# Optimization experiments

Hardware: AMD Instinct MI355X
Metric: run time of the kernel (lower is better)

## Reference

```python
import jax, jax.numpy as jnp
import numpy as np

B, C, H, W = 8, 256, 64, 64
NUM_HEADS = 4


def setup_inputs() -> dict:
    key = jax.random.key(0)
    ks = jax.random.split(key, 6)
    s = 0.02  # small init scale for 1x1 conv weights
    return {
        "x": jax.random.normal(ks[0], (B, C, H, W), jnp.float32),
        "cproj": jax.random.normal(ks[1], (B, C, H, W), jnp.float32),
        "wq": jax.random.normal(ks[2], (C, C), jnp.float32) * s,
        "bq": jnp.zeros((C,), jnp.float32),
        "wkv": jax.random.normal(ks[3], (2 * C, C), jnp.float32) * s,
        "bkv": jnp.zeros((2 * C,), jnp.float32),
        "wo": jax.random.normal(ks[4], (C, C), jnp.float32) * s,  # zero_module in torch; random here for a meaningful baseline
        "bo": jnp.zeros((C,), jnp.float32),
    }


def reference(x, cproj, wq, bq, wkv, bkv, wo, bo):
    Bb, Cc, Hh, Ww = x.shape
    N = Hh * Ww
    h = NUM_HEADS
    d = Cc // h
    scale = 1.0 / jnp.sqrt(jnp.sqrt(jnp.asarray(Cc, jnp.float32)))

    xf = x.reshape(Bb, Cc, N)
    cf = cproj.reshape(Bb, Cc, N)

    # 1x1 convs == channel matmuls
    Q = jnp.einsum('oc,bcn->bon', wq, xf) + bq[None, :, None]           # (B,C,N)
    KV = jnp.einsum('oc,bcn->bon', wkv, cf) + bkv[None, :, None]        # (B,2C,N)
    K, V = KV[:, :Cc], KV[:, Cc:]

    # softmax over channel-dim-within-head for q, over spatial N for k
    q = jax.nn.softmax(Q.reshape(Bb, h, d, N) * scale, axis=2).reshape(Bb, Cc, N)
    k = jax.nn.softmax(K.reshape(Bb, h, d, N), axis=3).reshape(Bb, Cc, N)

    # linear-attention: (B,C,C) context, then project back to N — note heads are mixed, per original bmm
    context = jnp.einsum('bcn,bdn->bcd', k, V)
    out = jnp.einsum('bcd,bdn->bcn', context, q)

    out = jnp.einsum('oc,bcn->bon', wo, out) + bo[None, :, None]
    return out.reshape(Bb, Cc, Hh, Ww)
```

## Files before the change

kernel.cpp:

```cpp
#include <hip/hip_runtime.h>

#define B_ 8
#define C_ 256
#define N_ 4096
#define NSPLIT 16

typedef float f32x4 __attribute__((ext_vector_type(4)));
typedef __bf16 bf16x8 __attribute__((ext_vector_type(8)));
typedef __bf16 bf16x4 __attribute__((ext_vector_type(4)));
typedef unsigned short u16x8 __attribute__((ext_vector_type(8)));
typedef unsigned short u16x4 __attribute__((ext_vector_type(4)));

__device__ __forceinline__ unsigned short f2bf(float f) {
  return __builtin_bit_cast(unsigned short, (__bf16)f);
}
__device__ __forceinline__ float bf2f(unsigned short u) {
  return __uint_as_float((unsigned)u << 16);
}

__device__ __forceinline__ f32x4 mfma16(bf16x8 a, bf16x8 b, f32x4 c) {
  return __builtin_amdgcn_mfma_f32_16x16x32_bf16(a, b, c, 0, 0, 0);
}

typedef __attribute__((address_space(1))) const void* gvp;
typedef __attribute__((address_space(3))) void* lvp;
__device__ __forceinline__ void gld16(const void* g, void* l) {
  __builtin_amdgcn_global_load_lds((gvp)g, (lvp)l, 16, 0, 0);
}

#define VMWAIT(N) do { asm volatile("s_waitcnt vmcnt(" #N ")" ::: "memory"); \
                       __builtin_amdgcn_sched_barrier(0); } while (0)
#define BAR() __builtin_amdgcn_s_barrier()

template <int ROWS>
__device__ __forceinline__ void stage(unsigned short* lds, const unsigned short* g,
                                      int ld, int w, int lane) {
  const int r8 = lane >> 3;
  const int ce = ((lane & 7) ^ r8) << 3;
  const unsigned short* gp = g + (size_t)(w * (ROWS / 4) + r8) * ld + ce;
  unsigned short* lp = lds + w * (ROWS / 4) * 64;
#pragma unroll
  for (int i = 0; i < ROWS / 32; i++)
    gld16(gp + (size_t)(i * 8) * ld, lp + i * 512);
}

__device__ __forceinline__ bf16x8 frag(const unsigned short* lds, int row, int kc) {
  return *(const bf16x8*)(lds + row * 64 + ((kc ^ (row & 7)) << 3));
}

__device__ __forceinline__ void loadB(float4* pbv, const float* src, int ld,
                                      int n0, int kt, int w, int lane) {
  const int nf = lane & 15, kg = lane >> 4;
  const float* sp = src + (size_t)(kt * 64 + w * 16 + kg * 4) * ld + n0 + 4 * nf;
#pragma unroll
  for (int h = 0; h < 2; h++)
#pragma unroll
    for (int i = 0; i < 4; i++)
      pbv[h * 4 + i] = *(const float4*)(sp + h * 64 + (size_t)i * ld);
}
__device__ __forceinline__ void writeB(unsigned short* Bs, const float4* pbv,
                                       int w, int lane) {
  const int nf = lane & 15, kg = lane >> 4;
  const int k0 = w * 16 + kg * 4;
#pragma unroll
  for (int h = 0; h < 2; h++)
#pragma unroll
    for (int j = 0; j < 4; j++) {
      bf16x4 o = (bf16x4){(__bf16)((const float*)&pbv[h * 4 + 0])[j],
                          (__bf16)((const float*)&pbv[h * 4 + 1])[j],
                          (__bf16)((const float*)&pbv[h * 4 + 2])[j],
                          (__bf16)((const float*)&pbv[h * 4 + 3])[j]};
      *(bf16x4*)&Bs[(h * 64 + 4 * nf + j) * 68 + k0] = o;
    }
}
__device__ __forceinline__ bf16x8 fragB(const unsigned short* Bs, int n, int k8) {
  union { u16x4 q[2]; bf16x8 b; } u;
  const unsigned short* p = Bs + n * 68 + k8 * 8;
  u.q[0] = *(const u16x4*)p;
  u.q[1] = *(const u16x4*)(p + 4);
  return u.b;
}

__device__ __forceinline__ bf16x8 fragC(const unsigned short* Ct, int n, int k8) {
  union { u16x4 q[2]; bf16x8 b; } u;
  const unsigned short* p = Ct + n * 268 + k8 * 8;
  u.q[0] = *(const u16x4*)p;
  u.q[1] = *(const u16x4*)(p + 4);
  return u.b;
}

__global__ __launch_bounds__(256) void castw(
    const float* __restrict__ wq, const float* __restrict__ wkv,
    const float* __restrict__ wo, unsigned short* __restrict__ wqb,
    unsigned short* __restrict__ wkvb, unsigned short* __restrict__ wob,
    float* __restrict__ Z) {
  int t = blockIdx.x * 256 + threadIdx.x;
  if (t < B_ * C_) Z[t] = 0.f;
  int i = t * 4;
  const float* src;
  unsigned short* dst;
  int off;
  if (i < 65536) { src = wq; dst = wqb; off = i; }
  else if (i < 196608) { src = wkv; dst = wkvb; off = i - 65536; }
  else { src = wo; dst = wob; off = i - 196608; }
  float4 v = *(const float4*)(src + off);
  *(u16x4*)(dst + off) = (u16x4){f2bf(v.x), f2bf(v.y), f2bf(v.z), f2bf(v.w)};
}

__device__ __forceinline__ void qproj_body(
    unsigned short* As, unsigned short* Bs, const unsigned short* __restrict__ wqb,
    const float* __restrict__ x, const float* __restrict__ bq,
    unsigned short* __restrict__ qT, int b, int n0, int m0b) {
  const int tid = threadIdx.x, lane = tid & 63, w = tid >> 6;
  const int m0w = (w >> 1) * 64;
  const int n0w = (w & 1) * 64;
  const int colL = lane & 15, kq = lane >> 4, quad = lane >> 4;
  const float* xb = x + (size_t)b * C_ * N_;

  f32x4 acc[4][4];
#pragma unroll
  for (int i = 0; i < 4; i++)
#pragma unroll
    for (int j = 0; j < 4; j++) acc[i][j] = (f32x4){0.f, 0.f, 0.f, 0.f};

  float4 pbv[8];
  loadB(pbv, xb, N_, n0, 0, w, lane);

  for (int kt = 0; kt < 4; kt++) {
    writeB(Bs, pbv, w, lane);
    stage<128>(As, wqb + (size_t)m0b * C_ + kt * 64, C_, w, lane);
    __syncthreads();
    if (kt < 3) loadB(pbv, xb, N_, n0, kt + 1, w, lane);
#pragma unroll
    for (int ks = 0; ks < 2; ks++) {
      bf16x8 af[4], bf[4];
#pragma unroll
      for (int mt = 0; mt < 4; mt++) af[mt] = frag(As, m0w + mt * 16 + colL, ks * 4 + kq);
#pragma unroll
      for (int nt = 0; nt < 4; nt++) bf[nt] = fragB(Bs, n0w + nt * 16 + colL, ks * 4 + kq);
#pragma unroll
      for (int mt = 0; mt < 4; mt++)
#pragma unroll
        for (int nt = 0; nt < 4; nt++) acc[mt][nt] = mfma16(af[mt], bf[nt], acc[mt][nt]);
    }
    __syncthreads();
  }

#pragma unroll
  for (int nt = 0; nt < 4; nt++) {
    float v[16];
    float mx = -1e30f;
#pragma unroll
    for (int mt = 0; mt < 4; mt++)
#pragma unroll
      for (int r = 0; r < 4; r++) {
        int m = m0b + m0w + mt * 16 + quad * 4 + r;
        float val = (acc[mt][nt][r] + bq[m]) * 0.25f;
        v[mt * 4 + r] = val;
        mx = fmaxf(mx, val);
      }
    mx = fmaxf(mx, __shfl_xor(mx, 16));
    mx = fmaxf(mx, __shfl_xor(mx, 32));
    float s = 0.f;
#pragma unroll
    for (int j = 0; j < 16; j++) { v[j] = __expf(v[j] - mx); s += v[j]; }
    s += __shfl_xor(s, 16);
    s += __shfl_xor(s, 32);
    float inv = 1.0f / s;
    const int n = n0 + n0w + nt * 16 + colL;
    unsigned short* qb = qT + ((size_t)b * N_ + n) * C_ + m0b + m0w;
#pragma unroll
    for (int mt = 0; mt < 4; mt++) {
      u16x4 o = (u16x4){f2bf(v[mt * 4 + 0] * inv), f2bf(v[mt * 4 + 1] * inv),
                        f2bf(v[mt * 4 + 2] * inv), f2bf(v[mt * 4 + 3] * inv)};
      *(u16x4*)(qb + mt * 16 + quad * 4) = o;
    }
  }
}

__device__ __forceinline__ void kvproj_body(
    unsigned short* As, unsigned short* Bs, const unsigned short* __restrict__ wkvb,
    const float* __restrict__ cp, const float* __restrict__ bkv,
    unsigned short* __restrict__ Eb, unsigned short* __restrict__ Vb,
    float* __restrict__ Z, int b, int n0, int m0b) {
  const int tid = threadIdx.x, lane = tid & 63, w = tid >> 6;
  const int m0w = w * 32;
  const int colL = lane & 15, kq = lane >> 4, quad = lane >> 4;
  const float* cpb = cp + (size_t)b * C_ * N_;

  f32x4 acc[2][8];
#pragma unroll
  for (int i = 0; i < 2; i++)
#pragma unroll
    for (int j = 0; j < 8; j++) acc[i][j] = (f32x4){0.f, 0.f, 0.f, 0.f};

  float4 pbv[8];
  loadB(pbv, cpb, N_, n0, 0, w, lane);

  for (int kt = 0; kt < 4; kt++) {
    writeB(Bs, pbv, w, lane);
    stage<128>(As, wkvb + (size_t)m0b * C_ + kt * 64, C_, w, lane);
    __syncthreads();
    if (kt < 3) loadB(pbv, cpb, N_, n0, kt + 1, w, lane);
#pragma unroll
    for (int ks = 0; ks < 2; ks++) {
      bf16x8 bf[8];
#pragma unroll
      for (int nt = 0; nt < 8; nt++) bf[nt] = fragB(Bs, nt * 16 + colL, ks * 4 + kq);
#pragma unroll
      for (int mt = 0; mt < 2; mt++) {
        bf16x8 af = frag(As, m0w + mt * 16 + colL, ks * 4 + kq);
#pragma unroll
        for (int nt = 0; nt < 8; nt++) acc[mt][nt] = mfma16(af, bf[nt], acc[mt][nt]);
      }
    }
    __syncthreads();
  }

#pragma unroll
  for (int mt = 0; mt < 2; mt++)
#pragma unroll
    for (int r = 0; r < 4; r++) {
      int m = m0b + m0w + mt * 16 + quad * 4 + r;
      float bias = bkv[m];
      if (m < C_) {
        unsigned short* er = Eb + ((size_t)b * C_ + m) * N_ + n0;
        float es = 0.f;
#pragma unroll
        for (int nt = 0; nt < 8; nt++) {
          float e = __expf(acc[mt][nt][r] + bias);
          er[nt * 16 + colL] = f2bf(e);
          es += e;
        }
        es += __shfl_xor(es, 1);
        es += __shfl_xor(es, 2);
        es += __shfl_xor(es, 4);
        es += __shfl_xor(es, 8);
        if ((lane & 15) == 0) atomicAdd(&Z[b * C_ + m], es);
      } else {
        unsigned short* vr = Vb + ((size_t)b * C_ + m - C_) * N_ + n0;
#pragma unroll
        for (int nt = 0; nt < 8; nt++) vr[nt * 16 + colL] = f2bf(acc[mt][nt][r] + bias);
      }
    }
}

__global__ __launch_bounds__(256) void qkvproj(
    const unsigned short* __restrict__ wqb, const unsigned short* __restrict__ wkvb,
    const float* __restrict__ x, const float* __restrict__ cp,
    const float* __restrict__ bq, const float* __restrict__ bkv,
    unsigned short* __restrict__ qT, unsigned short* __restrict__ Eb,
    unsigned short* __restrict__ Vb, float* __restrict__ Z) {
  __shared__ __align__(16) unsigned short As[128 * 64];
  __shared__ __align__(16) unsigned short Bs[128 * 68];
  const int b = blockIdx.z, n0 = blockIdx.x * 128;
  if (blockIdx.y < 2)
    qproj_body(As, Bs, wqb, x, bq, qT, b, n0, blockIdx.y * 128);
  else
    kvproj_body(As, Bs, wkvb, cp, bkv, Eb, Vb, Z, b, n0, (blockIdx.y - 2) * 128);
}

__global__ __launch_bounds__(256) void ctx_part(
    const unsigned short* __restrict__ Eb, const float* __restrict__ Z,
    const unsigned short* __restrict__ Vb, unsigned short* __restrict__ ctxp) {
  __shared__ __align__(16) unsigned short As[2][128 * 64];
  __shared__ __align__(16) unsigned short Bs[2][128 * 64];
  const int bid = blockIdx.x;
  const int swz = (bid & 7) * 64 + (bid >> 3);
  const int b = swz >> 6, r = swz & 63;
  const int s = r >> 2;
  const int m0 = ((r >> 1) & 1) * 128, n0 = (r & 1) * 128;
  const int tid = threadIdx.x, lane = tid & 63, w = tid >> 6;
  const int m0w = (w & 1) * 64, n0w = (w >> 1) * 64;
  const int colL = lane & 15, kq = lane >> 4, quad = lane >> 4;
  const unsigned short* Ag = Eb + ((size_t)b * C_ + m0) * N_ + s * (N_ / NSPLIT);
  const unsigned short* Bg = Vb + ((size_t)b * C_ + n0) * N_ + s * (N_ / NSPLIT);

  f32x4 acc[4][4];
#pragma unroll
  for (int i = 0; i < 4; i++)
#pragma unroll
    for (int j = 0; j < 4; j++) acc[i][j] = (f32x4){0.f, 0.f, 0.f, 0.f};

  stage<128>(As[0], Ag + 0 * 64, N_, w, lane);
  stage<128>(Bs[0], Bg + 0 * 64, N_, w, lane);
  stage<128>(As[1], Ag + 1 * 64, N_, w, lane);
  stage<128>(Bs[1], Bg + 1 * 64, N_, w, lane);
  VMWAIT(8);
  BAR();

  for (int kt = 0; kt < 4; kt++) {
    const unsigned short* Asc = As[kt & 1];
    const unsigned short* Bsc = Bs[kt & 1];
#pragma unroll
    for (int ks = 0; ks < 2; ks++) {
      bf16x8 af[4], bf[4];
#pragma unroll
      for (int mt = 0; mt < 4; mt++) af[mt] = frag(Asc, m0w + mt * 16 + colL, ks * 4 + kq);
#pragma unroll
      for (int nt = 0; nt < 4; nt++) bf[nt] = frag(Bsc, n0w + nt * 16 + colL, ks * 4 + kq);
#pragma unroll
      for (int mt = 0; mt < 4; mt++)
#pragma unroll
        for (int nt = 0; nt < 4; nt++) acc[mt][nt] = mfma16(af[mt], bf[nt], acc[mt][nt]);
    }
    if (kt == 3) break;
    BAR();
    if (kt + 2 < 4) {
      stage<128>(As[kt & 1], Ag + (kt + 2) * 64, N_, w, lane);
      stage<128>(Bs[kt & 1], Bg + (kt + 2) * 64, N_, w, lane);
      VMWAIT(8);
    } else {
      VMWAIT(0);
    }
    BAR();
  }

  unsigned short* outp = ctxp + ((size_t)s * B_ + b) * C_ * C_;
  const float* Zb = Z + b * C_;
#pragma unroll
  for (int mt = 0; mt < 4; mt++)
#pragma unroll
    for (int r2 = 0; r2 < 4; r2++) {
      int m = m0 + m0w + mt * 16 + quad * 4 + r2;
      float iz = 1.0f / Zb[m];
#pragma unroll
      for (int nt = 0; nt < 4; nt++) {
        int n = n0 + n0w + nt * 16 + colL;
        outp[(size_t)m * C_ + n] = f2bf(acc[mt][nt][r2] * iz);
      }
    }
}

__global__ __launch_bounds__(256) void ctxoproj(
    const unsigned short* __restrict__ ctxp, const unsigned short* __restrict__ wob,
    unsigned short* __restrict__ ctx2) {
  __shared__ __align__(16) unsigned short AsW[4 * 64 * 64];
  __shared__ __align__(16) unsigned short Ct[32 * 268];
  const int bid = blockIdx.x;
  const int swz = (bid & 7) * 32 + (bid >> 3);
  const int b = swz >> 5, r = swz & 31;
  const int o0 = (r >> 3) * 64, d0 = (r & 7) * 32;
  const int tid = threadIdx.x, lane = tid & 63, w = tid >> 6;
  const int colL = lane & 15, kq = lane >> 4, quad = lane >> 4;

#pragma unroll
  for (int ck = 0; ck < 4; ck++)
    stage<64>(AsW + ck * 4096, wob + (size_t)o0 * C_ + ck * 64, C_, w, lane);

  const int q = tid & 7, cl = tid >> 3;
  const unsigned short* pb = ctxp + ((size_t)b * C_ + cl) * C_ + d0 + q * 4;
#pragma unroll 2
  for (int p = 0; p < 8; p++) {
    f32x4 s4 = (f32x4){0.f, 0.f, 0.f, 0.f};
    const unsigned short* pp = pb + (size_t)p * 32 * C_;
#pragma unroll
    for (int s = 0; s < NSPLIT; s++) {
      u16x4 v = *(const u16x4*)(pp + (size_t)s * B_ * C_ * C_);
      s4[0] += bf2f(v[0]); s4[1] += bf2f(v[1]);
      s4[2] += bf2f(v[2]); s4[3] += bf2f(v[3]);
    }
    const int c = p * 32 + cl;
#pragma unroll
    for (int j = 0; j < 4; j++) Ct[(q * 4 + j) * 268 + c] = f2bf(s4[j]);
  }
  __syncthreads();

  f32x4 acc2[2];
  acc2[0] = (f32x4){0.f, 0.f, 0.f, 0.f};
  acc2[1] = (f32x4){0.f, 0.f, 0.f, 0.f};
#pragma unroll
  for (int kt = 0; kt < 4; kt++)
#pragma unroll
    for (int ks = 0; ks < 2; ks++) {
      bf16x8 af = frag(AsW + kt * 4096, w * 16 + colL, ks * 4 + kq);
#pragma unroll
      for (int nt = 0; nt < 2; nt++) {
        bf16x8 bf = fragC(Ct, nt * 16 + colL, kt * 8 + ks * 4 + kq);
        acc2[nt] = mfma16(af, bf, acc2[nt]);
      }
    }
  unsigned short* ob = ctx2 + (size_t)b * C_ * C_;
#pragma unroll
  for (int nt = 0; nt < 2; nt++)
#pragma unroll
    for (int r2 = 0; r2 < 4; r2++)
      ob[(size_t)(o0 + w * 16 + quad * 4 + r2) * C_ + d0 + nt * 16 + colL] =
          f2bf(acc2[nt][r2]);
}

__global__ __launch_bounds__(256) void outgemm(
    const unsigned short* __restrict__ ctx2, const unsigned short* __restrict__ qT,
    const float* __restrict__ bo, float* __restrict__ out) {
  __shared__ __align__(16) unsigned short As[2][128 * 64];
  __shared__ __align__(16) unsigned short Bs[2][64 * 64];
  const int bid = blockIdx.x;
  const int swz = (bid & 7) * 128 + (bid >> 3);
  const int b = swz >> 7, r = swz & 127;
  const int m0b = (r >> 6) * 128, n0 = (r & 63) * 64;
  const int tid = threadIdx.x, lane = tid & 63, w = tid >> 6;
  const int m0w = w * 32;
  const int colL = lane & 15, kq = lane >> 4, quad = lane >> 4;
  const unsigned short* Ag = ctx2 + (size_t)b * C_ * C_ + (size_t)m0b * C_;
  const unsigned short* Bg = qT + ((size_t)b * N_ + n0) * C_;

  f32x4 acc[2][4];
#pragma unroll
  for (int i = 0; i < 2; i++)
#pragma unroll
    for (int j = 0; j < 4; j++) acc[i][j] = (f32x4){0.f, 0.f, 0.f, 0.f};

  stage<128>(As[0], Ag + 0 * 64, C_, w, lane);
  stage<64>(Bs[0], Bg + 0 * 64, C_, w, lane);
  stage<128>(As[1], Ag + 1 * 64, C_, w, lane);
  stage<64>(Bs[1], Bg + 1 * 64, C_, w, lane);
  VMWAIT(6);
  BAR();

  for (int kt = 0; kt < 4; kt++) {
    const unsigned short* Asc = As[kt & 1];
    const unsigned short* Bsc = Bs[kt & 1];
#pragma unroll
    for (int ks = 0; ks < 2; ks++) {
      bf16x8 af[2], bf[4];
#pragma unroll
      for (int mt = 0; mt < 2; mt++) af[mt] = frag(Asc, m0w + mt * 16 + colL, ks * 4 + kq);
#pragma unroll
      for (int nt = 0; nt < 4; nt++) bf[nt] = frag(Bsc, nt * 16 + colL, ks * 4 + kq);
#pragma unroll
      for (int mt = 0; mt < 2; mt++)
#pragma unroll
        for (int nt = 0; nt < 4; nt++) acc[mt][nt] = mfma16(af[mt], bf[nt], acc[mt][nt]);
    }
    if (kt == 3) break;
    BAR();
    if (kt + 2 < 4) {
      stage<128>(As[kt & 1], Ag + (kt + 2) * 64, C_, w, lane);
      stage<64>(Bs[kt & 1], Bg + (kt + 2) * 64, C_, w, lane);
      VMWAIT(6);
    } else {
      VMWAIT(0);
    }
    BAR();
  }

  float* ob = out + (size_t)b * C_ * N_;
#pragma unroll
  for (int mt = 0; mt < 2; mt++)
#pragma unroll
    for (int r2 = 0; r2 < 4; r2++) {
      int m = m0b + m0w + mt * 16 + quad * 4 + r2;
      float bias = bo[m];
#pragma unroll
      for (int nt = 0; nt < 4; nt++) {
        int n = n0 + nt * 16 + colL;
        ob[(size_t)m * N_ + n] = acc[mt][nt][r2] + bias;
      }
    }
}

extern "C" void kernel_launch(void* const* d_in, const int* in_sizes, int n_in,
                              void* d_out, int out_size, void* d_ws, size_t ws_size,
                              hipStream_t stream) {
  const float* x     = (const float*)d_in[0];
  const float* cproj = (const float*)d_in[1];
  const float* wq    = (const float*)d_in[2];
  const float* bq    = (const float*)d_in[3];
  const float* wkv   = (const float*)d_in[4];
  const float* bkv   = (const float*)d_in[5];
  const float* wo    = (const float*)d_in[6];
  const float* bo    = (const float*)d_in[7];
  float* out = (float*)d_out;

  unsigned short* qT    = (unsigned short*)d_ws;
  unsigned short* Eb    = qT + 8388608;
  unsigned short* Vb    = Eb + 8388608;
  unsigned short* ctxp  = Vb + 8388608;
  unsigned short* wqb   = ctxp + 8388608;
  unsigned short* wkvb  = wqb + 65536;
  unsigned short* wob   = wkvb + 131072;
  unsigned short* ctx2  = wob + 65536;
  float*          Zbuf  = (float*)(ctx2 + 524288);

  castw<<<256, 256, 0, stream>>>(wq, wkv, wo, wqb, wkvb, wob, Zbuf);
  qkvproj<<<dim3(32, 6, 8), 256, 0, stream>>>(wqb, wkvb, x, cproj, bq, bkv,
                                              qT, Eb, Vb, Zbuf);
  ctx_part<<<512, 256, 0, stream>>>(Eb, Zbuf, Vb, ctxp);
  ctxoproj<<<256, 256, 0, stream>>>(ctxp, wob, ctx2);
  outgemm<<<1024, 256, 0, stream>>>(ctx2, qT, bo, out);
}
```

Measured before the change: 181.4 us.

## Move Q projection into the context kernel to overlap with ctx partials

Splits the fused QKV projection launch into a KV-only projection and a new kernel that runs the context partial GEMM blocks alongside the Q projection blocks. The goal is to fill the GPU during the context stage, which has only 512 blocks, with the independent Q projection work, and to shorten the KV kernel. In exchange the ctx body gives up its double-buffered async staging for a simple single-buffer loop with syncthreads, so it shares the same LDS footprint with qproj. The B-tile LDS pitch also changes from 68 to 70 to alter the bank-conflict pattern.

```diff
diff --git a/kernel.cpp b/kernel.cpp
--- a/kernel.cpp
+++ b/kernel.cpp
@@ -48,6 +48,7 @@
   return *(const bf16x8*)(lds + row * 64 + ((kc ^ (row & 7)) << 3));
 }
 
+#define BPITCH 70
 __device__ __forceinline__ void loadB(float4* pbv, const float* src, int ld,
                                       int n0, int kt, int w, int lane) {
   const int nf = lane & 15, kg = lane >> 4;
@@ -70,12 +71,12 @@
                           (__bf16)((const float*)&pbv[h * 4 + 1])[j],
                           (__bf16)((const float*)&pbv[h * 4 + 2])[j],
                           (__bf16)((const float*)&pbv[h * 4 + 3])[j]};
-      *(bf16x4*)&Bs[(h * 64 + 4 * nf + j) * 68 + k0] = o;
+      *(bf16x4*)&Bs[(h * 64 + 4 * nf + j) * BPITCH + k0] = o;
     }
 }
 __device__ __forceinline__ bf16x8 fragB(const unsigned short* Bs, int n, int k8) {
   union { u16x4 q[2]; bf16x8 b; } u;
-  const unsigned short* p = Bs + n * 68 + k8 * 8;
+  const unsigned short* p = Bs + n * BPITCH + k8 * 8;
   u.q[0] = *(const u16x4*)p;
   u.q[1] = *(const u16x4*)(p + 4);
   return u.b;
@@ -107,77 +108,6 @@
   *(u16x4*)(dst + off) = (u16x4){f2bf(v.x), f2bf(v.y), f2bf(v.z), f2bf(v.w)};
 }
 
-__device__ __forceinline__ void qproj_body(
-    unsigned short* As, unsigned short* Bs, const unsigned short* __restrict__ wqb,
-    const float* __restrict__ x, const float* __restrict__ bq,
-    unsigned short* __restrict__ qT, int b, int n0, int m0b) {
-  const int tid = threadIdx.x, lane = tid & 63, w = tid >> 6;
-  const int m0w = (w >> 1) * 64;
-  const int n0w = (w & 1) * 64;
-  const int colL = lane & 15, kq = lane >> 4, quad = lane >> 4;
-  const float* xb = x + (size_t)b * C_ * N_;
-
-  f32x4 acc[4][4];
-#pragma unroll
-  for (int i = 0; i < 4; i++)
-#pragma unroll
-    for (int j = 0; j < 4; j++) acc[i][j] = (f32x4){0.f, 0.f, 0.f, 0.f};
-
-  float4 pbv[8];
-  loadB(pbv, xb, N_, n0, 0, w, lane);
-
-  for (int kt = 0; kt < 4; kt++) {
-    writeB(Bs, pbv, w, lane);
-    stage<128>(As, wqb + (size_t)m0b * C_ + kt * 64, C_, w, lane);
-    __syncthreads();
-    if (kt < 3) loadB(pbv, xb, N_, n0, kt + 1, w, lane);
-#pragma unroll
-    for (int ks = 0; ks < 2; ks++) {
-      bf16x8 af[4], bf[4];
-#pragma unroll
-      for (int mt = 0; mt < 4; mt++) af[mt] = frag(As, m0w + mt * 16 + colL, ks * 4 + kq);
-#pragma unroll
-      for (int nt = 0; nt < 4; nt++) bf[nt] = fragB(Bs, n0w + nt * 16 + colL, ks * 4 + kq);
-#pragma unroll
-      for (int mt = 0; mt < 4; mt++)
-#pragma unroll
-        for (int nt = 0; nt < 4; nt++) acc[mt][nt] = mfma16(af[mt], bf[nt], acc[mt][nt]);
-    }
-    __syncthreads();
-  }
-
-#pragma unroll
-  for (int nt = 0; nt < 4; nt++) {
-    float v[16];
-    float mx = -1e30f;
-#pragma unroll
-    for (int mt = 0; mt < 4; mt++)
-#pragma unroll
-      for (int r = 0; r < 4; r++) {
-        int m = m0b + m0w + mt * 16 + quad * 4 + r;
-        float val = (acc[mt][nt][r] + bq[m]) * 0.25f;
-        v[mt * 4 + r] = val;
-        mx = fmaxf(mx, val);
-      }
-    mx = fmaxf(mx, __shfl_xor(mx, 16));
-    mx = fmaxf(mx, __shfl_xor(mx, 32));
-    float s = 0.f;
-#pragma unroll
-    for (int j = 0; j < 16; j++) { v[j] = __expf(v[j] - mx); s += v[j]; }
-    s += __shfl_xor(s, 16);
-    s += __shfl_xor(s, 32);
-    float inv = 1.0f / s;
-    const int n = n0 + n0w + nt * 16 + colL;
-    unsigned short* qb = qT + ((size_t)b * N_ + n) * C_ + m0b + m0w;
-#pragma unroll
-    for (int mt = 0; mt < 4; mt++) {
-      u16x4 o = (u16x4){f2bf(v[mt * 4 + 0] * inv), f2bf(v[mt * 4 + 1] * inv),
-                        f2bf(v[mt * 4 + 2] * inv), f2bf(v[mt * 4 + 3] * inv)};
-      *(u16x4*)(qb + mt * 16 + quad * 4) = o;
-    }
-  }
-}
-
 __device__ __forceinline__ void kvproj_body(
     unsigned short* As, unsigned short* Bs, const unsigned short* __restrict__ wkvb,
     const float* __restrict__ cp, const float* __restrict__ bkv,
@@ -245,31 +175,91 @@
     }
 }
 
-__global__ __launch_bounds__(256) void qkvproj(
-    const unsigned short* __restrict__ wqb, const unsigned short* __restrict__ wkvb,
-    const float* __restrict__ x, const float* __restrict__ cp,
-    const float* __restrict__ bq, const float* __restrict__ bkv,
-    unsigned short* __restrict__ qT, unsigned short* __restrict__ Eb,
+__global__ __launch_bounds__(256) void kvproj(
+    const unsigned short* __restrict__ wkvb, const float* __restrict__ cp,
+    const float* __restrict__ bkv, unsigned short* __restrict__ Eb,
     unsigned short* __restrict__ Vb, float* __restrict__ Z) {
   __shared__ __align__(16) unsigned short As[128 * 64];
-  __shared__ __align__(16) unsigned short Bs[128 * 68];
-  const int b = blockIdx.z, n0 = blockIdx.x * 128;
-  if (blockIdx.y < 2)
-    qproj_body(As, Bs, wqb, x, bq, qT, b, n0, blockIdx.y * 128);
-  else
-    kvproj_body(As, Bs, wkvb, cp, bkv, Eb, Vb, Z, b, n0, (blockIdx.y - 2) * 128);
-}
-
-__global__ __launch_bounds__(256) void ctx_part(
-    const unsigned short* __restrict__ Eb, const float* __restrict__ Z,
-    const unsigned short* __restrict__ Vb, unsigned short* __restrict__ ctxp) {
-  __shared__ __align__(16) unsigned short As[2][128 * 64];
-  __shared__ __align__(16) unsigned short Bs[2][128 * 64];
-  const int bid = blockIdx.x;
-  const int swz = (bid & 7) * 64 + (bid >> 3);
-  const int b = swz >> 6, r = swz & 63;
-  const int s = r >> 2;
-  const int m0 = ((r >> 1) & 1) * 128, n0 = (r & 1) * 128;
+  __shared__ __align__(16) unsigned short Bs[128 * BPITCH];
+  kvproj_body(As, Bs, wkvb, cp, bkv, Eb, Vb, Z,
+              blockIdx.z, blockIdx.x * 128, blockIdx.y * 128);
+}
+
+__device__ __forceinline__ void qproj_body(
+    unsigned short* As, unsigned short* Bs, const unsigned short* __restrict__ wqb,
+    const float* __restrict__ x, const float* __restrict__ bq,
+    unsigned short* __restrict__ qT, int b, int n0, int m0b) {
+  const int tid = threadIdx.x, lane = tid & 63, w = tid >> 6;
+  const int m0w = (w >> 1) * 64;
+  const int n0w = (w & 1) * 64;
+  const int colL = lane & 15, kq = lane >> 4, quad = lane >> 4;
+  const float* xb = x + (size_t)b * C_ * N_;
+
+  f32x4 acc[4][4];
+#pragma unroll
+  for (int i = 0; i < 4; i++)
+#pragma unroll
+    for (int j = 0; j < 4; j++) acc[i][j] = (f32x4){0.f, 0.f, 0.f, 0.f};
+
+  float4 pbv[8];
+  loadB(pbv, xb, N_, n0, 0, w, lane);
+
+  for (int kt = 0; kt < 4; kt++) {
+    writeB(Bs, pbv, w, lane);
+    stage<128>(As, wqb + (size_t)m0b * C_ + kt * 64, C_, w, lane);
+    __syncthreads();
+    if (kt < 3) loadB(pbv, xb, N_, n0, kt + 1, w, lane);
+#pragma unroll
+    for (int ks = 0; ks < 2; ks++) {
+      bf16x8 af[4], bf[4];
+#pragma unroll
+      for (int mt = 0; mt < 4; mt++) af[mt] = frag(As, m0w + mt * 16 + colL, ks * 4 + kq);
+#pragma unroll
+      for (int nt = 0; nt < 4; nt++) bf[nt] = fragB(Bs, n0w + nt * 16 + colL, ks * 4 + kq);
+#pragma unroll
+      for (int mt = 0; mt < 4; mt++)
+#pragma unroll
+        for (int nt = 0; nt < 4; nt++) acc[mt][nt] = mfma16(af[mt], bf[nt], acc[mt][nt]);
+    }
+    __syncthreads();
+  }
+
+#pragma unroll
+  for (int nt = 0; nt < 4; nt++) {
+    float v[16];
+    float mx = -1e30f;
+#pragma unroll
+    for (int mt = 0; mt < 4; mt++)
+#pragma unroll
+      for (int r = 0; r < 4; r++) {
+        int m = m0b + m0w + mt * 16 + quad * 4 + r;
+        float val = (acc[mt][nt][r] + bq[m]) * 0.25f;
+        v[mt * 4 + r] = val;
+        mx = fmaxf(mx, val);
+      }
+    mx = fmaxf(mx, __shfl_xor(mx, 16));
+    mx = fmaxf(mx, __shfl_xor(mx, 32));
+    float s = 0.f;
+#pragma unroll
+    for (int j = 0; j < 16; j++) { v[j] = __expf(v[j] - mx); s += v[j]; }
+    s += __shfl_xor(s, 16);
+    s += __shfl_xor(s, 32);
+    float inv = 1.0f / s;
+    const int n = n0 + n0w + nt * 16 + colL;
+    unsigned short* qb = qT + ((size_t)b * N_ + n) * C_ + m0b + m0w;
+#pragma unroll
+    for (int mt = 0; mt < 4; mt++) {
+      u16x4 o = (u16x4){f2bf(v[mt * 4 + 0] * inv), f2bf(v[mt * 4 + 1] * inv),
+                        f2bf(v[mt * 4 + 2] * inv), f2bf(v[mt * 4 + 3] * inv)};
+      *(u16x4*)(qb + mt * 16 + quad * 4) = o;
+    }
+  }
+}
+
+__device__ __forceinline__ void ctx_body(
+    unsigned short* As, unsigned short* Bs, const unsigned short* __restrict__ Eb,
+    const float* __restrict__ Z, const unsigned short* __restrict__ Vb,
+    unsigned short* __restrict__ ctxp, int b, int s, int m0, int n0) {
   const int tid = threadIdx.x, lane = tid & 63, w = tid >> 6;
   const int m0w = (w & 1) * 64, n0w = (w >> 1) * 64;
   const int colL = lane & 15, kq = lane >> 4, quad = lane >> 4;
@@ -282,38 +272,23 @@
 #pragma unroll
     for (int j = 0; j < 4; j++) acc[i][j] = (f32x4){0.f, 0.f, 0.f, 0.f};
 
-  stage<128>(As[0], Ag + 0 * 64, N_, w, lane);
-  stage<128>(Bs[0], Bg + 0 * 64, N_, w, lane);
-  stage<128>(As[1], Ag + 1 * 64, N_, w, lane);
-  stage<128>(Bs[1], Bg + 1 * 64, N_, w, lane);
-  VMWAIT(8);
-  BAR();
-
-  for (int kt = 0; kt < 4; kt++) {
-    const unsigned short* Asc = As[kt & 1];
-    const unsigned short* Bsc = Bs[kt & 1];
+  for (int kt = 0; kt < (N_ / NSPLIT) / 64; kt++) {
+    stage<128>(As, Ag + kt * 64, N_, w, lane);
+    stage<128>(Bs, Bg + kt * 64, N_, w, lane);
+    __syncthreads();
 #pragma unroll
     for (int ks = 0; ks < 2; ks++) {
       bf16x8 af[4], bf[4];
 #pragma unroll
-      for (int mt = 0; mt < 4; mt++) af[mt] = frag(Asc, m0w + mt * 16 + colL, ks * 4 + kq);
-#pragma unroll
-      for (int nt = 0; nt < 4; nt++) bf[nt] = frag(Bsc, n0w + nt * 16 + colL, ks * 4 + kq);
+      for (int mt = 0; mt < 4; mt++) af[mt] = frag(As, m0w + mt * 16 + colL, ks * 4 + kq);
+#pragma unroll
+      for (int nt = 0; nt < 4; nt++) bf[nt] = frag(Bs, n0w + nt * 16 + colL, ks * 4 + kq);
 #pragma unroll
       for (int mt = 0; mt < 4; mt++)
 #pragma unroll
         for (int nt = 0; nt < 4; nt++) acc[mt][nt] = mfma16(af[mt], bf[nt], acc[mt][nt]);
     }
-    if (kt == 3) break;
-    BAR();
-    if (kt + 2 < 4) {
-      stage<128>(As[kt & 1], Ag + (kt + 2) * 64, N_, w, lane);
-      stage<128>(Bs[kt & 1], Bg + (kt + 2) * 64, N_, w, lane);
-      VMWAIT(8);
-    } else {
-      VMWAIT(0);
-    }
-    BAR();
+    __syncthreads();
   }
 
   unsigned short* outp = ctxp + ((size_t)s * B_ + b) * C_ * C_;
@@ -330,6 +305,25 @@
         outp[(size_t)m * C_ + n] = f2bf(acc[mt][nt][r2] * iz);
       }
     }
+}
+
+__global__ __launch_bounds__(256) void qproj_ctx(
+    const unsigned short* __restrict__ wqb, const float* __restrict__ x,
+    const float* __restrict__ bq, unsigned short* __restrict__ qT,
+    const unsigned short* __restrict__ Eb, const float* __restrict__ Z,
+    const unsigned short* __restrict__ Vb, unsigned short* __restrict__ ctxp) {
+  __shared__ __align__(16) unsigned short As[128 * 64];
+  __shared__ __align__(16) unsigned short Bs[128 * BPITCH];
+  const int id = blockIdx.x;
+  if (id < 512) {
+    const int swz = (id & 7) * 64 + (id >> 3);
+    const int b = swz >> 6, r = swz & 63;
+    ctx_body(As, Bs, Eb, Z, Vb, ctxp, b, r >> 2, ((r >> 1) & 1) * 128, (r & 1) * 128);
+  } else {
+    const int qid = id - 512;
+    const int j = qid >> 8, p = qid & 255;
+    qproj_body(As, Bs, wqb, x, bq, qT, p >> 5, (p & 31) * 128, j * 128);
+  }
 }
 
 __global__ __launch_bounds__(256) void ctxoproj(
@@ -483,9 +477,8 @@
   float*          Zbuf  = (float*)(ctx2 + 524288);
 
   castw<<<256, 256, 0, stream>>>(wq, wkv, wo, wqb, wkvb, wob, Zbuf);
-  qkvproj<<<dim3(32, 6, 8), 256, 0, stream>>>(wqb, wkvb, x, cproj, bq, bkv,
-                                              qT, Eb, Vb, Zbuf);
-  ctx_part<<<512, 256, 0, stream>>>(Eb, Zbuf, Vb, ctxp);
+  kvproj<<<dim3(32, 4, 8), 256, 0, stream>>>(wkvb, cproj, bkv, Eb, Vb, Zbuf);
+  qproj_ctx<<<1024, 256, 0, stream>>>(wqb, x, bq, qT, Eb, Zbuf, Vb, ctxp);
   ctxoproj<<<256, 256, 0, stream>>>(ctxp, wob, ctx2);
   outgemm<<<1024, 256, 0, stream>>>(ctx2, qT, bo, out);
 }
```

After: 239.0 us. +31.7%, slower.
